# Kernel optimization log

Measured on AMD Instinct MI355X. Metric: run time of the kernel, lower is better.

## Reference

```python
import jax, jax.numpy as jnp
import numpy as np

# Serving-scale prefill: 4 seqs x 512 tokens, GQA 16q/4kv heads, 128 head_dim,
# flat paged KV cache with 131072 slots (pages*block_size).
N = 2048
HQ = 16
HKV = 4
D = 128
NUM_SLOTS = 131072
SEQ = 512
SCALE = 1.0 / float(np.sqrt(D))  # matches init scale


def setup_inputs() -> dict:
    key = jax.random.key(0)
    kq, kk, kv, ks = jax.random.split(key, 4)
    q = jax.random.normal(kq, (N, HQ, D), jnp.float32)
    k = jax.random.normal(kk, (N, HKV, D), jnp.float32)
    v = jax.random.normal(kv, (N, HKV, D), jnp.float32)
    k_cache = jnp.zeros((NUM_SLOTS, HKV * D), jnp.float32)
    v_cache = jnp.zeros((NUM_SLOTS, HKV * D), jnp.float32)
    # distinct slots (no write collisions), like a real page allocator
    slot_mapping = jax.random.permutation(ks, NUM_SLOTS)[:N].astype(jnp.int32)
    cu_seqlens = jnp.arange(0, N + 1, SEQ, dtype=jnp.int32)  # [0,512,...,2048]
    return {"q": q, "k": k, "v": v, "k_cache": k_cache, "v_cache": v_cache,
            "slot_mapping": slot_mapping, "cu_seqlens": cu_seqlens}


def reference(q, k, v, k_cache, v_cache, slot_mapping, cu_seqlens):
    n = q.shape[0]
    # --- store_kvcache: parallel scatter keyed by slot_mapping, -1 dropped ---
    safe = jnp.where(slot_mapping >= 0, slot_mapping, NUM_SLOTS)  # OOB -> drop
    k_cache = k_cache.at[safe].set(k.reshape(n, HKV * D), mode="drop")
    v_cache = v_cache.at[safe].set(v.reshape(n, HKV * D), mode="drop")

    # --- paged read: gather this step's KV back from the cache (block_table path) ---
    read = jnp.clip(slot_mapping, 0, NUM_SLOTS - 1)
    kc = k_cache[read].reshape(n, HKV, D)
    vc = v_cache[read].reshape(n, HKV, D)

    # --- varlen causal attention (flash_attn_varlen_func equivalent) ---
    pos = jnp.arange(n)
    seg = jnp.searchsorted(cu_seqlens, pos, side="right") - 1  # segment id per token
    group = HQ // HKV
    ke = jnp.repeat(kc, group, axis=1)  # [N, HQ, D]
    ve = jnp.repeat(vc, group, axis=1)
    scores = jnp.einsum("qhd,khd->hqk", q, ke) * jnp.asarray(SCALE, q.dtype)
    mask = (seg[:, None] == seg[None, :]) & (pos[None, :] <= pos[:, None])  # [N,N]
    neg = jnp.asarray(jnp.finfo(scores.dtype).min, scores.dtype)
    scores = jnp.where(mask[None, :, :], scores, neg)
    p = jax.nn.softmax(scores, axis=-1)
    o = jnp.einsum("hqk,khd->qhd", p, ve)  # [N, HQ, D]
    return o
```

## Files before the change

### kernel.cpp

```cpp
#include <hip/hip_runtime.h>

#define N_TOK 2048
#define HQ_ 16
#define HKV_ 4
#define D_ 128
#define NUM_SLOTS_ 131072
#define SEQ_ 512
#define NSEG_ 4
#define KVS (HKV_ * D_)

typedef __attribute__((ext_vector_type(8))) short bf16x8;
typedef __attribute__((ext_vector_type(4))) float f32x4;
typedef __attribute__((ext_vector_type(4))) short s16x4;

__device__ __forceinline__ unsigned cvt_pk(float lo, float hi) {
  unsigned r;
  asm("v_cvt_pk_bf16_f32 %0, %1, %2" : "=v"(r) : "v"(lo), "v"(hi));
  return r;
}
union bfu { bf16x8 v; unsigned u[4]; };

__global__ __launch_bounds__(256) void prep_kernel(
    const float* __restrict__ k, const float* __restrict__ v,
    const float* __restrict__ k_cache, const float* __restrict__ v_cache,
    const int* __restrict__ slot_mapping,
    short* __restrict__ k_bf, short* __restrict__ vt) {
  __shared__ short tile[16][64];
  int b = blockIdx.x;
  if (b < 1024) {
    int e = (b * 256 + (int)threadIdx.x) * 4;
    int n = e >> 9;
    int s = slot_mapping[n];
    bool valid = (s >= 0) && (s < NUM_SLOTS_);
    int cs = s < 0 ? 0 : (s >= NUM_SLOTS_ ? NUM_SLOTS_ - 1 : s);
    const float* src = valid ? (k + e)
                             : (k_cache + (size_t)cs * KVS + (e & (KVS - 1)));
    f32x4 a = *(const f32x4*)src;
    int seg = n >> 9, tok = n & (SEQ_ - 1);
    int h = (e >> 7) & 3, d = e & 127;
    unsigned* dst = (unsigned*)(k_bf + ((size_t)((seg * HKV_ + h) * SEQ_ + tok)) * D_ + d);
    dst[0] = cvt_pk(a[0], a[1]);
    dst[1] = cvt_pk(a[2], a[3]);
  } else {
    int bb = b - 1024;
    int dblk = bb & 7, h = (bb >> 3) & 3, seg = (bb >> 5) & 3, ch = (bb >> 7) & 7;
    int d0 = dblk * 16;
    const int tid = (int)threadIdx.x;
    int tok_l = tid >> 2, dq = tid & 3;
    int n = seg * SEQ_ + ch * 64 + tok_l;
    int s = slot_mapping[n];
    bool valid = (s >= 0) && (s < NUM_SLOTS_);
    int cs = s < 0 ? 0 : (s >= NUM_SLOTS_ ? NUM_SLOTS_ - 1 : s);
    const float* src = (valid ? v + (size_t)n * KVS : v_cache + (size_t)cs * KVS)
                       + h * D_ + d0 + dq * 4;
    f32x4 x = *(const f32x4*)src;
#pragma unroll
    for (int j = 0; j < 4; ++j) tile[dq * 4 + j][tok_l] = (short)cvt_pk(x[j], x[j]);
    __syncthreads();
    int d_l = tid >> 4, tq = tid & 15;
    s16x4 o = *(const s16x4*)&tile[d_l][tq * 4];
    short* dst = vt + ((size_t)((seg * HKV_ + h) * D_ + d0 + d_l)) * SEQ_ + ch * 64 + tq * 4;
    *(s16x4*)dst = o;
  }
}

__global__ __launch_bounds__(256) void attn_kernel(
    const float* __restrict__ q, const short* __restrict__ k_bf,
    const short* __restrict__ vt, float* __restrict__ out) {
  __shared__ float sm_o[3][2][8][64][4];
  __shared__ float sm_l[3][2][64];
  const int tid = (int)threadIdx.x;
  const int wave = tid >> 6;
  const int lane = tid & 63;
  const int col = lane & 15;
  const int grp = lane >> 4;
  const int p = (int)blockIdx.x;
  const int xcd = p & 7;
  const int local = p >> 3;
  const int g = xcd * 2 + (local >> 5);
  const int h2 = (local >> 3) & 3;
  const int j = local & 7;
  const int seg = g >> 2;
  const int kvh = g & 3;
  const int head = kvh * 4 + h2;
  const int segbase = seg * SEQ_;
  const float MLOG = 11.5415603f;
  const short* ksegb = k_bf + (size_t)(seg * HKV_ + kvh) * SEQ_ * D_ + (size_t)col * D_ + grp * 8;
  const short* vseg = vt + ((size_t)((seg * HKV_ + kvh) * D_ + col)) * SEQ_ + grp * 8;
  const int srcA = col + ((grp & 1) << 5);
  const int srcB = srcA + 16;
  const bool lo2 = grp < 2;

#pragma unroll 1
  for (int ti = 0; ti < 2; ++ti) {
    const int qt32 = ti ? j : (15 - j);
    const int q0 = qt32 << 5;

    bf16x8 qfA[4], qfB[4];
    {
      const float sc = 0.12751742f;
      const float* qpA = q + ((size_t)((segbase + q0 + col) * HQ_ + head)) * D_ + grp * 8;
      const float* qpB = qpA + (size_t)16 * HQ_ * D_;
#pragma unroll
      for (int t = 0; t < 4; ++t) {
        f32x4 a = *(const f32x4*)(qpA + t * 32);
        f32x4 bb = *(const f32x4*)(qpA + t * 32 + 4);
        bfu f;
        f.u[0] = cvt_pk(a[0] * sc, a[1] * sc);
        f.u[1] = cvt_pk(a[2] * sc, a[3] * sc);
        f.u[2] = cvt_pk(bb[0] * sc, bb[1] * sc);
        f.u[3] = cvt_pk(bb[2] * sc, bb[3] * sc);
        qfA[t] = f.v;
        a = *(const f32x4*)(qpB + t * 32);
        bb = *(const f32x4*)(qpB + t * 32 + 4);
        f.u[0] = cvt_pk(a[0] * sc, a[1] * sc);
        f.u[1] = cvt_pk(a[2] * sc, a[3] * sc);
        f.u[2] = cvt_pk(bb[0] * sc, bb[1] * sc);
        f.u[3] = cvt_pk(bb[2] * sc, bb[3] * sc);
        qfB[t] = f.v;
      }
    }

    f32x4 oA[8], oB[8];
#pragma unroll
    for (int t = 0; t < 8; ++t) { oA[t] = (f32x4){0,0,0,0}; oB[t] = (f32x4){0,0,0,0}; }
    float lA = 0.f, lB = 0.f;
    const int nfull = q0 >> 5;

    for (int blk = wave; blk < nfull; blk += 4) {
      const int k0 = blk << 5;
      const short* kp = ksegb + (size_t)k0 * D_;
      f32x4 sA0 = {0,0,0,0}, sA1 = {0,0,0,0}, sB0 = {0,0,0,0}, sB1 = {0,0,0,0};
#pragma unroll
      for (int t = 0; t < 4; ++t) {
        bf16x8 kf0 = *(const bf16x8*)(kp + t * 32);
        bf16x8 kf1 = *(const bf16x8*)(kp + 16 * D_ + t * 32);
        sA0 = __builtin_amdgcn_mfma_f32_16x16x32_bf16(kf0, qfA[t], sA0, 0, 0, 0);
        sA1 = __builtin_amdgcn_mfma_f32_16x16x32_bf16(kf1, qfA[t], sA1, 0, 0, 0);
        sB0 = __builtin_amdgcn_mfma_f32_16x16x32_bf16(kf0, qfB[t], sB0, 0, 0, 0);
        sB1 = __builtin_amdgcn_mfma_f32_16x16x32_bf16(kf1, qfB[t], sB1, 0, 0, 0);
      }
#pragma unroll
      for (int r = 0; r < 4; ++r) {
        sA0[r] = __builtin_amdgcn_exp2f(sA0[r] - MLOG);
        sA1[r] = __builtin_amdgcn_exp2f(sA1[r] - MLOG);
        sB0[r] = __builtin_amdgcn_exp2f(sB0[r] - MLOG);
        sB1[r] = __builtin_amdgcn_exp2f(sB1[r] - MLOG);
        lA += sA0[r] + sA1[r];
        lB += sB0[r] + sB1[r];
      }
      bfu pfA, pfB;
      {
        unsigned u0 = cvt_pk(sA0[0], sA0[1]), u1 = cvt_pk(sA0[2], sA0[3]);
        unsigned u2 = cvt_pk(sA1[0], sA1[1]), u3 = cvt_pk(sA1[2], sA1[3]);
        int a0 = __shfl((int)u0, srcA, 64), a1 = __shfl((int)u1, srcA, 64);
        int a2 = __shfl((int)u2, srcA, 64), a3 = __shfl((int)u3, srcA, 64);
        int b0 = __shfl((int)u0, srcB, 64), b1 = __shfl((int)u1, srcB, 64);
        int b2 = __shfl((int)u2, srcB, 64), b3 = __shfl((int)u3, srcB, 64);
        pfA.u[0] = lo2 ? a0 : a2; pfA.u[1] = lo2 ? a1 : a3;
        pfA.u[2] = lo2 ? b0 : b2; pfA.u[3] = lo2 ? b1 : b3;
        u0 = cvt_pk(sB0[0], sB0[1]); u1 = cvt_pk(sB0[2], sB0[3]);
        u2 = cvt_pk(sB1[0], sB1[1]); u3 = cvt_pk(sB1[2], sB1[3]);
        a0 = __shfl((int)u0, srcA, 64); a1 = __shfl((int)u1, srcA, 64);
        a2 = __shfl((int)u2, srcA, 64); a3 = __shfl((int)u3, srcA, 64);
        b0 = __shfl((int)u0, srcB, 64); b1 = __shfl((int)u1, srcB, 64);
        b2 = __shfl((int)u2, srcB, 64); b3 = __shfl((int)u3, srcB, 64);
        pfB.u[0] = lo2 ? a0 : a2; pfB.u[1] = lo2 ? a1 : a3;
        pfB.u[2] = lo2 ? b0 : b2; pfB.u[3] = lo2 ? b1 : b3;
      }
      const short* vp = vseg + k0;
#pragma unroll
      for (int t = 0; t < 8; ++t) {
        bf16x8 vf = *(const bf16x8*)(vp + (size_t)(t * 16) * SEQ_);
        oA[t] = __builtin_amdgcn_mfma_f32_16x16x32_bf16(vf, pfA.v, oA[t], 0, 0, 0);
        oB[t] = __builtin_amdgcn_mfma_f32_16x16x32_bf16(vf, pfB.v, oB[t], 0, 0, 0);
      }
    }

    if ((nfull & 3) == wave) {
      const int k0 = q0;
      const short* kp = ksegb + (size_t)k0 * D_;
      f32x4 sA0 = {0,0,0,0}, sB0 = {0,0,0,0}, sB1 = {0,0,0,0};
#pragma unroll
      for (int t = 0; t < 4; ++t) {
        bf16x8 kf0 = *(const bf16x8*)(kp + t * 32);
        bf16x8 kf1 = *(const bf16x8*)(kp + 16 * D_ + t * 32);
        sA0 = __builtin_amdgcn_mfma_f32_16x16x32_bf16(kf0, qfA[t], sA0, 0, 0, 0);
        sB0 = __builtin_amdgcn_mfma_f32_16x16x32_bf16(kf0, qfB[t], sB0, 0, 0, 0);
        sB1 = __builtin_amdgcn_mfma_f32_16x16x32_bf16(kf1, qfB[t], sB1, 0, 0, 0);
      }
      f32x4 sA1 = {0, 0, 0, 0};
#pragma unroll
      for (int r = 0; r < 4; ++r) {
        bool msk = (grp * 4 + r) > col;
        float pa0 = __builtin_amdgcn_exp2f(sA0[r] - MLOG);
        float pb1 = __builtin_amdgcn_exp2f(sB1[r] - MLOG);
        sA0[r] = msk ? 0.f : pa0;
        sB0[r] = __builtin_amdgcn_exp2f(sB0[r] - MLOG);
        sB1[r] = msk ? 0.f : pb1;
        lA += sA0[r];
        lB += sB0[r] + sB1[r];
      }
      bfu pfA, pfB;
      {
        unsigned u0 = cvt_pk(sA0[0], sA0[1]), u1 = cvt_pk(sA0[2], sA0[3]);
        unsigned u2 = cvt_pk(sA1[0], sA1[1]), u3 = cvt_pk(sA1[2], sA1[3]);
        int a0 = __shfl((int)u0, srcA, 64), a1 = __shfl((int)u1, srcA, 64);
        int a2 = __shfl((int)u2, srcA, 64), a3 = __shfl((int)u3, srcA, 64);
        int b0 = __shfl((int)u0, srcB, 64), b1 = __shfl((int)u1, srcB, 64);
        int b2 = __shfl((int)u2, srcB, 64), b3 = __shfl((int)u3, srcB, 64);
        pfA.u[0] = lo2 ? a0 : a2; pfA.u[1] = lo2 ? a1 : a3;
        pfA.u[2] = lo2 ? b0 : b2; pfA.u[3] = lo2 ? b1 : b3;
        u0 = cvt_pk(sB0[0], sB0[1]); u1 = cvt_pk(sB0[2], sB0[3]);
        u2 = cvt_pk(sB1[0], sB1[1]); u3 = cvt_pk(sB1[2], sB1[3]);
        a0 = __shfl((int)u0, srcA, 64); a1 = __shfl((int)u1, srcA, 64);
        a2 = __shfl((int)u2, srcA, 64); a3 = __shfl((int)u3, srcA, 64);
        b0 = __shfl((int)u0, srcB, 64); b1 = __shfl((int)u1, srcB, 64);
        b2 = __shfl((int)u2, srcB, 64); b3 = __shfl((int)u3, srcB, 64);
        pfB.u[0] = lo2 ? a0 : a2; pfB.u[1] = lo2 ? a1 : a3;
        pfB.u[2] = lo2 ? b0 : b2; pfB.u[3] = lo2 ? b1 : b3;
      }
      const short* vp = vseg + k0;
#pragma unroll
      for (int t = 0; t < 8; ++t) {
        bf16x8 vf = *(const bf16x8*)(vp + (size_t)(t * 16) * SEQ_);
        oA[t] = __builtin_amdgcn_mfma_f32_16x16x32_bf16(vf, pfA.v, oA[t], 0, 0, 0);
        oB[t] = __builtin_amdgcn_mfma_f32_16x16x32_bf16(vf, pfB.v, oB[t], 0, 0, 0);
      }
    }

    lA += __shfl_xor(lA, 16); lA += __shfl_xor(lA, 32);
    lB += __shfl_xor(lB, 16); lB += __shfl_xor(lB, 32);

    __syncthreads();
    if (wave) {
#pragma unroll
      for (int t = 0; t < 8; ++t) {
        *(f32x4*)&sm_o[wave - 1][0][t][lane][0] = oA[t];
        *(f32x4*)&sm_o[wave - 1][1][t][lane][0] = oB[t];
      }
      sm_l[wave - 1][0][lane] = lA;
      sm_l[wave - 1][1][lane] = lB;
    }
    __syncthreads();
    if (!wave) {
      float ltotA = lA + sm_l[0][0][lane] + sm_l[1][0][lane] + sm_l[2][0][lane];
      float ltotB = lB + sm_l[0][1][lane] + sm_l[1][1][lane] + sm_l[2][1][lane];
      float linvA = 1.0f / ltotA;
      float linvB = 1.0f / ltotB;
      float* opA = out + ((size_t)((segbase + q0 + col) * HQ_ + head)) * D_ + grp * 4;
      float* opB = opA + (size_t)16 * HQ_ * D_;
#pragma unroll
      for (int t = 0; t < 8; ++t) {
        f32x4 rA = oA[t], rB = oB[t];
#pragma unroll
        for (int w = 0; w < 3; ++w) {
          rA += *(const f32x4*)&sm_o[w][0][t][lane][0];
          rB += *(const f32x4*)&sm_o[w][1][t][lane][0];
        }
        rA *= linvA;
        rB *= linvB;
        *(f32x4*)(opA + t * 16) = rA;
        *(f32x4*)(opB + t * 16) = rB;
      }
    }
  }
}

extern "C" void kernel_launch(void* const* d_in, const int* in_sizes, int n_in,
                              void* d_out, int out_size, void* d_ws, size_t ws_size,
                              hipStream_t stream) {
  const float* q = (const float*)d_in[0];
  const float* k = (const float*)d_in[1];
  const float* v = (const float*)d_in[2];
  const float* k_cache = (const float*)d_in[3];
  const float* v_cache = (const float*)d_in[4];
  const int* slot_mapping = (const int*)d_in[5];

  short* k_bf = (short*)d_ws;
  short* vt = k_bf + (size_t)N_TOK * HKV_ * D_;

  prep_kernel<<<2048, 256, 0, stream>>>(k, v, k_cache, v_cache, slot_mapping, k_bf, vt);
  attn_kernel<<<512, 256, 0, stream>>>(q, k_bf, vt, (float*)d_out);
}
```

Measured before the change: 38.69 us.

## Run both causal query tiles concurrently in 512-thread blocks

Instead of looping serially over the two balanced query tiles (15-j and j) with 4 waves, each block now has 8 waves, and each group of 4 waves handles one tile at the same time. The cross-wave reduction is split into two phases (A rows then B rows) to halve the shared-memory buffer per quad, adding extra barriers. Launch bounds change to 512 threads with a minimum of 4 blocks per CU, which may limit registers per thread and cause spills. The quad handling the longer tile still determines block latency, so the gain relies on the serial second pass being removed.

Measured after the change: 48.05 us. 24.2% more time.

```diff
diff --git a/kernel.cpp b/kernel.cpp
--- a/kernel.cpp
+++ b/kernel.cpp
@@ -64,13 +64,15 @@
   }
 }
 
-__global__ __launch_bounds__(256) void attn_kernel(
+__global__ __launch_bounds__(512, 4) void attn_kernel(
     const float* __restrict__ q, const short* __restrict__ k_bf,
     const short* __restrict__ vt, float* __restrict__ out) {
-  __shared__ float sm_o[3][2][8][64][4];
-  __shared__ float sm_l[3][2][64];
+  __shared__ float sm_o[2][3][8][64][4];
+  __shared__ float sm_l[2][3][2][64];
   const int tid = (int)threadIdx.x;
   const int wave = tid >> 6;
+  const int quad = wave >> 2;
+  const int wq = wave & 3;
   const int lane = tid & 63;
   const int col = lane & 15;
   const int grp = lane >> 4;
@@ -91,178 +93,182 @@
   const int srcB = srcA + 16;
   const bool lo2 = grp < 2;
 
-#pragma unroll 1
-  for (int ti = 0; ti < 2; ++ti) {
-    const int qt32 = ti ? j : (15 - j);
-    const int q0 = qt32 << 5;
-
-    bf16x8 qfA[4], qfB[4];
+  const int qt32 = quad ? j : (15 - j);
+  const int q0 = qt32 << 5;
+
+  bf16x8 qfA[4], qfB[4];
+  {
+    const float sc = 0.12751742f;
+    const float* qpA = q + ((size_t)((segbase + q0 + col) * HQ_ + head)) * D_ + grp * 8;
+    const float* qpB = qpA + (size_t)16 * HQ_ * D_;
+#pragma unroll
+    for (int t = 0; t < 4; ++t) {
+      f32x4 a = *(const f32x4*)(qpA + t * 32);
+      f32x4 bb = *(const f32x4*)(qpA + t * 32 + 4);
+      bfu f;
+      f.u[0] = cvt_pk(a[0] * sc, a[1] * sc);
+      f.u[1] = cvt_pk(a[2] * sc, a[3] * sc);
+      f.u[2] = cvt_pk(bb[0] * sc, bb[1] * sc);
+      f.u[3] = cvt_pk(bb[2] * sc, bb[3] * sc);
+      qfA[t] = f.v;
+      a = *(const f32x4*)(qpB + t * 32);
+      bb = *(const f32x4*)(qpB + t * 32 + 4);
+      f.u[0] = cvt_pk(a[0] * sc, a[1] * sc);
+      f.u[1] = cvt_pk(a[2] * sc, a[3] * sc);
+      f.u[2] = cvt_pk(bb[0] * sc, bb[1] * sc);
+      f.u[3] = cvt_pk(bb[2] * sc, bb[3] * sc);
+      qfB[t] = f.v;
+    }
+  }
+
+  f32x4 oA[8], oB[8];
+#pragma unroll
+  for (int t = 0; t < 8; ++t) { oA[t] = (f32x4){0,0,0,0}; oB[t] = (f32x4){0,0,0,0}; }
+  float lA = 0.f, lB = 0.f;
+  const int nfull = q0 >> 5;
+
+  for (int blk = wq; blk < nfull; blk += 4) {
+    const int k0 = blk << 5;
+    const short* kp = ksegb + (size_t)k0 * D_;
+    f32x4 sA0 = {0,0,0,0}, sA1 = {0,0,0,0}, sB0 = {0,0,0,0}, sB1 = {0,0,0,0};
+#pragma unroll
+    for (int t = 0; t < 4; ++t) {
+      bf16x8 kf0 = *(const bf16x8*)(kp + t * 32);
+      bf16x8 kf1 = *(const bf16x8*)(kp + 16 * D_ + t * 32);
+      sA0 = __builtin_amdgcn_mfma_f32_16x16x32_bf16(kf0, qfA[t], sA0, 0, 0, 0);
+      sA1 = __builtin_amdgcn_mfma_f32_16x16x32_bf16(kf1, qfA[t], sA1, 0, 0, 0);
+      sB0 = __builtin_amdgcn_mfma_f32_16x16x32_bf16(kf0, qfB[t], sB0, 0, 0, 0);
+      sB1 = __builtin_amdgcn_mfma_f32_16x16x32_bf16(kf1, qfB[t], sB1, 0, 0, 0);
+    }
+#pragma unroll
+    for (int r = 0; r < 4; ++r) {
+      sA0[r] = __builtin_amdgcn_exp2f(sA0[r] - MLOG);
+      sA1[r] = __builtin_amdgcn_exp2f(sA1[r] - MLOG);
+      sB0[r] = __builtin_amdgcn_exp2f(sB0[r] - MLOG);
+      sB1[r] = __builtin_amdgcn_exp2f(sB1[r] - MLOG);
+      lA += sA0[r] + sA1[r];
+      lB += sB0[r] + sB1[r];
+    }
+    bfu pfA, pfB;
     {
-      const float sc = 0.12751742f;
-      const float* qpA = q + ((size_t)((segbase + q0 + col) * HQ_ + head)) * D_ + grp * 8;
-      const float* qpB = qpA + (size_t)16 * HQ_ * D_;
-#pragma unroll
-      for (int t = 0; t < 4; ++t) {
-        f32x4 a = *(const f32x4*)(qpA + t * 32);
-        f32x4 bb = *(const f32x4*)(qpA + t * 32 + 4);
-        bfu f;
-        f.u[0] = cvt_pk(a[0] * sc, a[1] * sc);
-        f.u[1] = cvt_pk(a[2] * sc, a[3] * sc);
-        f.u[2] = cvt_pk(bb[0] * sc, bb[1] * sc);
-        f.u[3] = cvt_pk(bb[2] * sc, bb[3] * sc);
-        qfA[t] = f.v;
-        a = *(const f32x4*)(qpB + t * 32);
-        bb = *(const f32x4*)(qpB + t * 32 + 4);
-        f.u[0] = cvt_pk(a[0] * sc, a[1] * sc);
-        f.u[1] = cvt_pk(a[2] * sc, a[3] * sc);
-        f.u[2] = cvt_pk(bb[0] * sc, bb[1] * sc);
-        f.u[3] = cvt_pk(bb[2] * sc, bb[3] * sc);
-        qfB[t] = f.v;
-      }
-    }
-
-    f32x4 oA[8], oB[8];
-#pragma unroll
-    for (int t = 0; t < 8; ++t) { oA[t] = (f32x4){0,0,0,0}; oB[t] = (f32x4){0,0,0,0}; }
-    float lA = 0.f, lB = 0.f;
-    const int nfull = q0 >> 5;
-
-    for (int blk = wave; blk < nfull; blk += 4) {
-      const int k0 = blk << 5;
-      const short* kp = ksegb + (size_t)k0 * D_;
-      f32x4 sA0 = {0,0,0,0}, sA1 = {0,0,0,0}, sB0 = {0,0,0,0}, sB1 = {0,0,0,0};
-#pragma unroll
-      for (int t = 0; t < 4; ++t) {
-        bf16x8 kf0 = *(const bf16x8*)(kp + t * 32);
-        bf16x8 kf1 = *(const bf16x8*)(kp + 16 * D_ + t * 32);
-        sA0 = __builtin_amdgcn_mfma_f32_16x16x32_bf16(kf0, qfA[t], sA0, 0, 0, 0);
-        sA1 = __builtin_amdgcn_mfma_f32_16x16x32_bf16(kf1, qfA[t], sA1, 0, 0, 0);
-        sB0 = __builtin_amdgcn_mfma_f32_16x16x32_bf16(kf0, qfB[t], sB0, 0, 0, 0);
-        sB1 = __builtin_amdgcn_mfma_f32_16x16x32_bf16(kf1, qfB[t], sB1, 0, 0, 0);
-      }
-#pragma unroll
-      for (int r = 0; r < 4; ++r) {
-        sA0[r] = __builtin_amdgcn_exp2f(sA0[r] - MLOG);
-        sA1[r] = __builtin_amdgcn_exp2f(sA1[r] - MLOG);
-        sB0[r] = __builtin_amdgcn_exp2f(sB0[r] - MLOG);
-        sB1[r] = __builtin_amdgcn_exp2f(sB1[r] - MLOG);
-        lA += sA0[r] + sA1[r];
-        lB += sB0[r] + sB1[r];
-      }
-      bfu pfA, pfB;
-      {
-        unsigned u0 = cvt_pk(sA0[0], sA0[1]), u1 = cvt_pk(sA0[2], sA0[3]);
-        unsigned u2 = cvt_pk(sA1[0], sA1[1]), u3 = cvt_pk(sA1[2], sA1[3]);
-        int a0 = __shfl((int)u0, srcA, 64), a1 = __shfl((int)u1, srcA, 64);
-        int a2 = __shfl((int)u2, srcA, 64), a3 = __shfl((int)u3, srcA, 64);
-        int b0 = __shfl((int)u0, srcB, 64), b1 = __shfl((int)u1, srcB, 64);
-        int b2 = __shfl((int)u2, srcB, 64), b3 = __shfl((int)u3, srcB, 64);
-        pfA.u[0] = lo2 ? a0 : a2; pfA.u[1] = lo2 ? a1 : a3;
-        pfA.u[2] = lo2 ? b0 : b2; pfA.u[3] = lo2 ? b1 : b3;
-        u0 = cvt_pk(sB0[0], sB0[1]); u1 = cvt_pk(sB0[2], sB0[3]);
-        u2 = cvt_pk(sB1[0], sB1[1]); u3 = cvt_pk(sB1[2], sB1[3]);
-        a0 = __shfl((int)u0, srcA, 64); a1 = __shfl((int)u1, srcA, 64);
-        a2 = __shfl((int)u2, srcA, 64); a3 = __shfl((int)u3, srcA, 64);
-        b0 = __shfl((int)u0, srcB, 64); b1 = __shfl((int)u1, srcB, 64);
-        b2 = __shfl((int)u2, srcB, 64); b3 = __shfl((int)u3, srcB, 64);
-        pfB.u[0] = lo2 ? a0 : a2; pfB.u[1] = lo2 ? a1 : a3;
-        pfB.u[2] = lo2 ? b0 : b2; pfB.u[3] = lo2 ? b1 : b3;
-      }
-      const short* vp = vseg + k0;
-#pragma unroll
-      for (int t = 0; t < 8; ++t) {
-        bf16x8 vf = *(const bf16x8*)(vp + (size_t)(t * 16) * SEQ_);
-        oA[t] = __builtin_amdgcn_mfma_f32_16x16x32_bf16(vf, pfA.v, oA[t], 0, 0, 0);
-        oB[t] = __builtin_amdgcn_mfma_f32_16x16x32_bf16(vf, pfB.v, oB[t], 0, 0, 0);
-      }
-    }
-
-    if ((nfull & 3) == wave) {
-      const int k0 = q0;
-      const short* kp = ksegb + (size_t)k0 * D_;
-      f32x4 sA0 = {0,0,0,0}, sB0 = {0,0,0,0}, sB1 = {0,0,0,0};
-#pragma unroll
-      for (int t = 0; t < 4; ++t) {
-        bf16x8 kf0 = *(const bf16x8*)(kp + t * 32);
-        bf16x8 kf1 = *(const bf16x8*)(kp + 16 * D_ + t * 32);
-        sA0 = __builtin_amdgcn_mfma_f32_16x16x32_bf16(kf0, qfA[t], sA0, 0, 0, 0);
-        sB0 = __builtin_amdgcn_mfma_f32_16x16x32_bf16(kf0, qfB[t], sB0, 0, 0, 0);
-        sB1 = __builtin_amdgcn_mfma_f32_16x16x32_bf16(kf1, qfB[t], sB1, 0, 0, 0);
-      }
-      f32x4 sA1 = {0, 0, 0, 0};
-#pragma unroll
-      for (int r = 0; r < 4; ++r) {
-        bool msk = (grp * 4 + r) > col;
-        float pa0 = __builtin_amdgcn_exp2f(sA0[r] - MLOG);
-        float pb1 = __builtin_amdgcn_exp2f(sB1[r] - MLOG);
-        sA0[r] = msk ? 0.f : pa0;
-        sB0[r] = __builtin_amdgcn_exp2f(sB0[r] - MLOG);
-        sB1[r] = msk ? 0.f : pb1;
-        lA += sA0[r];
-        lB += sB0[r] + sB1[r];
-      }
-      bfu pfA, pfB;
-      {
-        unsigned u0 = cvt_pk(sA0[0], sA0[1]), u1 = cvt_pk(sA0[2], sA0[3]);
-        unsigned u2 = cvt_pk(sA1[0], sA1[1]), u3 = cvt_pk(sA1[2], sA1[3]);
-        int a0 = __shfl((int)u0, srcA, 64), a1 = __shfl((int)u1, srcA, 64);
-        int a2 = __shfl((int)u2, srcA, 64), a3 = __shfl((int)u3, srcA, 64);
-        int b0 = __shfl((int)u0, srcB, 64), b1 = __shfl((int)u1, srcB, 64);
-        int b2 = __shfl((int)u2, srcB, 64), b3 = __shfl((int)u3, srcB, 64);
-        pfA.u[0] = lo2 ? a0 : a2; pfA.u[1] = lo2 ? a1 : a3;
-        pfA.u[2] = lo2 ? b0 : b2; pfA.u[3] = lo2 ? b1 : b3;
-        u0 = cvt_pk(sB0[0], sB0[1]); u1 = cvt_pk(sB0[2], sB0[3]);
-        u2 = cvt_pk(sB1[0], sB1[1]); u3 = cvt_pk(sB1[2], sB1[3]);
-        a0 = __shfl((int)u0, srcA, 64); a1 = __shfl((int)u1, srcA, 64);
-        a2 = __shfl((int)u2, srcA, 64); a3 = __shfl((int)u3, srcA, 64);
-        b0 = __shfl((int)u0, srcB, 64); b1 = __shfl((int)u1, srcB, 64);
-        b2 = __shfl((int)u2, srcB, 64); b3 = __shfl((int)u3, srcB, 64);
-        pfB.u[0] = lo2 ? a0 : a2; pfB.u[1] = lo2 ? a1 : a3;
-        pfB.u[2] = lo2 ? b0 : b2; pfB.u[3] = lo2 ? b1 : b3;
-      }
-      const short* vp = vseg + k0;
-#pragma unroll
-      for (int t = 0; t < 8; ++t) {
-        bf16x8 vf = *(const bf16x8*)(vp + (size_t)(t * 16) * SEQ_);
-        oA[t] = __builtin_amdgcn_mfma_f32_16x16x32_bf16(vf, pfA.v, oA[t], 0, 0, 0);
-        oB[t] = __builtin_amdgcn_mfma_f32_16x16x32_bf16(vf, pfB.v, oB[t], 0, 0, 0);
-      }
-    }
-
-    lA += __shfl_xor(lA, 16); lA += __shfl_xor(lA, 32);
-    lB += __shfl_xor(lB, 16); lB += __shfl_xor(lB, 32);
-
-    __syncthreads();
-    if (wave) {
-#pragma unroll
-      for (int t = 0; t < 8; ++t) {
-        *(f32x4*)&sm_o[wave - 1][0][t][lane][0] = oA[t];
-        *(f32x4*)&sm_o[wave - 1][1][t][lane][0] = oB[t];
-      }
-      sm_l[wave - 1][0][lane] = lA;
-      sm_l[wave - 1][1][lane] = lB;
-    }
-    __syncthreads();
-    if (!wave) {
-      float ltotA = lA + sm_l[0][0][lane] + sm_l[1][0][lane] + sm_l[2][0][lane];
-      float ltotB = lB + sm_l[0][1][lane] + sm_l[1][1][lane] + sm_l[2][1][lane];
-      float linvA = 1.0f / ltotA;
-      float linvB = 1.0f / ltotB;
-      float* opA = out + ((size_t)((segbase + q0 + col) * HQ_ + head)) * D_ + grp * 4;
-      float* opB = opA + (size_t)16 * HQ_ * D_;
-#pragma unroll
-      for (int t = 0; t < 8; ++t) {
-        f32x4 rA = oA[t], rB = oB[t];
-#pragma unroll
-        for (int w = 0; w < 3; ++w) {
-          rA += *(const f32x4*)&sm_o[w][0][t][lane][0];
-          rB += *(const f32x4*)&sm_o[w][1][t][lane][0];
-        }
-        rA *= linvA;
-        rB *= linvB;
-        *(f32x4*)(opA + t * 16) = rA;
-        *(f32x4*)(opB + t * 16) = rB;
-      }
+      unsigned u0 = cvt_pk(sA0[0], sA0[1]), u1 = cvt_pk(sA0[2], sA0[3]);
+      unsigned u2 = cvt_pk(sA1[0], sA1[1]), u3 = cvt_pk(sA1[2], sA1[3]);
+      int a0 = __shfl((int)u0, srcA, 64), a1 = __shfl((int)u1, srcA, 64);
+      int a2 = __shfl((int)u2, srcA, 64), a3 = __shfl((int)u3, srcA, 64);
+      int b0 = __shfl((int)u0, srcB, 64), b1 = __shfl((int)u1, srcB, 64);
+      int b2 = __shfl((int)u2, srcB, 64), b3 = __shfl((int)u3, srcB, 64);
+      pfA.u[0] = lo2 ? a0 : a2; pfA.u[1] = lo2 ? a1 : a3;
+      pfA.u[2] = lo2 ? b0 : b2; pfA.u[3] = lo2 ? b1 : b3;
+      u0 = cvt_pk(sB0[0], sB0[1]); u1 = cvt_pk(sB0[2], sB0[3]);
+      u2 = cvt_pk(sB1[0], sB1[1]); u3 = cvt_pk(sB1[2], sB1[3]);
+      a0 = __shfl((int)u0, srcA, 64); a1 = __shfl((int)u1, srcA, 64);
+      a2 = __shfl((int)u2, srcA, 64); a3 = __shfl((int)u3, srcA, 64);
+      b0 = __shfl((int)u0, srcB, 64); b1 = __shfl((int)u1, srcB, 64);
+      b2 = __shfl((int)u2, srcB, 64); b3 = __shfl((int)u3, srcB, 64);
+      pfB.u[0] = lo2 ? a0 : a2; pfB.u[1] = lo2 ? a1 : a3;
+      pfB.u[2] = lo2 ? b0 : b2; pfB.u[3] = lo2 ? b1 : b3;
+    }
+    const short* vp = vseg + k0;
+#pragma unroll
+    for (int t = 0; t < 8; ++t) {
+      bf16x8 vf = *(const bf16x8*)(vp + (size_t)(t * 16) * SEQ_);
+      oA[t] = __builtin_amdgcn_mfma_f32_16x16x32_bf16(vf, pfA.v, oA[t], 0, 0, 0);
+      oB[t] = __builtin_amdgcn_mfma_f32_16x16x32_bf16(vf, pfB.v, oB[t], 0, 0, 0);
+    }
+  }
+
+  if ((nfull & 3) == wq) {
+    const int k0 = q0;
+    const short* kp = ksegb + (size_t)k0 * D_;
+    f32x4 sA0 = {0,0,0,0}, sB0 = {0,0,0,0}, sB1 = {0,0,0,0};
+#pragma unroll
+    for (int t = 0; t < 4; ++t) {
+      bf16x8 kf0 = *(const bf16x8*)(kp + t * 32);
+      bf16x8 kf1 = *(const bf16x8*)(kp + 16 * D_ + t * 32);
+      sA0 = __builtin_amdgcn_mfma_f32_16x16x32_bf16(kf0, qfA[t], sA0, 0, 0, 0);
+      sB0 = __builtin_amdgcn_mfma_f32_16x16x32_bf16(kf0, qfB[t], sB0, 0, 0, 0);
+      sB1 = __builtin_amdgcn_mfma_f32_16x16x32_bf16(kf1, qfB[t], sB1, 0, 0, 0);
+    }
+    f32x4 sA1 = {0, 0, 0, 0};
+#pragma unroll
+    for (int r = 0; r < 4; ++r) {
+      bool msk = (grp * 4 + r) > col;
+      float pa0 = __builtin_amdgcn_exp2f(sA0[r] - MLOG);
+      float pb1 = __builtin_amdgcn_exp2f(sB1[r] - MLOG);
+      sA0[r] = msk ? 0.f : pa0;
+      sB0[r] = __builtin_amdgcn_exp2f(sB0[r] - MLOG);
+      sB1[r] = msk ? 0.f : pb1;
+      lA += sA0[r];
+      lB += sB0[r] + sB1[r];
+    }
+    bfu pfA, pfB;
+    {
+      unsigned u0 = cvt_pk(sA0[0], sA0[1]), u1 = cvt_pk(sA0[2], sA0[3]);
+      unsigned u2 = cvt_pk(sA1[0], sA1[1]), u3 = cvt_pk(sA1[2], sA1[3]);
+      int a0 = __shfl((int)u0, srcA, 64), a1 = __shfl((int)u1, srcA, 64);
+      int a2 = __shfl((int)u2, srcA, 64), a3 = __shfl((int)u3, srcA, 64);
+      int b0 = __shfl((int)u0, srcB, 64), b1 = __shfl((int)u1, srcB, 64);
+      int b2 = __shfl((int)u2, srcB, 64), b3 = __shfl((int)u3, srcB, 64);
+      pfA.u[0] = lo2 ? a0 : a2; pfA.u[1] = lo2 ? a1 : a3;
+      pfA.u[2] = lo2 ? b0 : b2; pfA.u[3] = lo2 ? b1 : b3;
+      u0 = cvt_pk(sB0[0], sB0[1]); u1 = cvt_pk(sB0[2], sB0[3]);
+      u2 = cvt_pk(sB1[0], sB1[1]); u3 = cvt_pk(sB1[2], sB1[3]);
+      a0 = __shfl((int)u0, srcA, 64); a1 = __shfl((int)u1, srcA, 64);
+      a2 = __shfl((int)u2, srcA, 64); a3 = __shfl((int)u3, srcA, 64);
+      b0 = __shfl((int)u0, srcB, 64); b1 = __shfl((int)u1, srcB, 64);
+      b2 = __shfl((int)u2, srcB, 64); b3 = __shfl((int)u3, srcB, 64);
+      pfB.u[0] = lo2 ? a0 : a2; pfB.u[1] = lo2 ? a1 : a3;
+      pfB.u[2] = lo2 ? b0 : b2; pfB.u[3] = lo2 ? b1 : b3;
+    }
+    const short* vp = vseg + k0;
+#pragma unroll
+    for (int t = 0; t < 8; ++t) {
+      bf16x8 vf = *(const bf16x8*)(vp + (size_t)(t * 16) * SEQ_);
+      oA[t] = __builtin_amdgcn_mfma_f32_16x16x32_bf16(vf, pfA.v, oA[t], 0, 0, 0);
+      oB[t] = __builtin_amdgcn_mfma_f32_16x16x32_bf16(vf, pfB.v, oB[t], 0, 0, 0);
+    }
+  }
+
+  lA += __shfl_xor(lA, 16); lA += __shfl_xor(lA, 32);
+  lB += __shfl_xor(lB, 16); lB += __shfl_xor(lB, 32);
+
+  if (wq) {
+#pragma unroll
+    for (int t = 0; t < 8; ++t) *(f32x4*)&sm_o[quad][wq - 1][t][lane][0] = oA[t];
+    sm_l[quad][wq - 1][0][lane] = lA;
+    sm_l[quad][wq - 1][1][lane] = lB;
+  }
+  __syncthreads();
+  if (!wq) {
+    float ltot = lA + sm_l[quad][0][0][lane] + sm_l[quad][1][0][lane] + sm_l[quad][2][0][lane];
+    float linv = 1.0f / ltot;
+    float* op = out + ((size_t)((segbase + q0 + col) * HQ_ + head)) * D_ + grp * 4;
+#pragma unroll
+    for (int t = 0; t < 8; ++t) {
+      f32x4 r = oA[t];
+#pragma unroll
+      for (int w = 0; w < 3; ++w) r += *(const f32x4*)&sm_o[quad][w][t][lane][0];
+      r *= linv;
+      *(f32x4*)(op + t * 16) = r;
+    }
+  }
+  __syncthreads();
+  if (wq) {
+#pragma unroll
+    for (int t = 0; t < 8; ++t) *(f32x4*)&sm_o[quad][wq - 1][t][lane][0] = oB[t];
+  }
+  __syncthreads();
+  if (!wq) {
+    float ltot = lB + sm_l[quad][0][1][lane] + sm_l[quad][1][1][lane] + sm_l[quad][2][1][lane];
+    float linv = 1.0f / ltot;
+    float* op = out + ((size_t)((segbase + q0 + 16 + col) * HQ_ + head)) * D_ + grp * 4;
+#pragma unroll
+    for (int t = 0; t < 8; ++t) {
+      f32x4 r = oB[t];
+#pragma unroll
+      for (int w = 0; w < 3; ++w) r += *(const f32x4*)&sm_o[quad][w][t][lane][0];
+      r *= linv;
+      *(f32x4*)(op + t * 16) = r;
     }
   }
 }
@@ -281,5 +287,5 @@
   short* vt = k_bf + (size_t)N_TOK * HKV_ * D_;
 
   prep_kernel<<<2048, 256, 0, stream>>>(k, v, k_cache, v_cache, slot_mapping, k_bf, vt);
-  attn_kernel<<<512, 256, 0, stream>>>(q, k_bf, vt, (float*)d_out);
-}
+  attn_kernel<<<512, 512, 0, stream>>>(q, k_bf, vt, (float*)d_out);
+}
```
